# Performance work log

Measured on AMD Instinct MI355X. Metric: run time of the kernel, lower is better.

The kernel has to match this reference:

```python
import jax, jax.numpy as jnp
import numpy as np

B, N = 256, 256


def greedy_hard_perm(soft_perm):
    # soft_perm: (B, N, N). Sequential greedy masked-argmax assignment, vectorized over batch.
    Bn, Nn, _ = soft_perm.shape
    NEG = jnp.finfo(soft_perm.dtype).min
    b_idx = jnp.arange(Bn)

    def step(carry, _):
        scores, hard, row_mask, col_mask = carry
        # mask out already-assigned rows/cols (in-place masked_fill_ in torch -> carried scores)
        scores = jnp.where(row_mask[:, :, None], NEG, scores)
        scores = jnp.where(col_mask[:, None, :], NEG, scores)
        flat_idx = jnp.argmax(scores.reshape(Bn, -1), axis=1)  # (B,)
        r = flat_idx // Nn
        c = flat_idx % Nn
        hard = hard.at[b_idx, r, c].set(1.0)
        row_mask = row_mask.at[b_idx, r].set(True)
        col_mask = col_mask.at[b_idx, c].set(True)
        return (scores, hard, row_mask, col_mask), None

    init = (
        soft_perm,
        jnp.zeros_like(soft_perm),
        jnp.zeros((Bn, Nn), dtype=bool),
        jnp.zeros((Bn, Nn), dtype=bool),
    )
    (_, hard, _, _), _ = jax.lax.scan(step, init, None, length=Nn)
    return hard


def setup_inputs() -> dict:
    key = jax.random.key(0)
    logits = jax.random.normal(key, (B, N, N), dtype=jnp.float32)
    # realistic soft permutation: row-stochastic scores
    soft_perm = jax.nn.softmax(logits, axis=-1)
    return {"soft_perm": soft_perm}


def reference(soft_perm):
    # hard perm carries no gradient (built from constant 1.0 writes in torch)
    hard = greedy_hard_perm(jax.lax.stop_gradient(soft_perm))
    # straight-through estimator: forward = hard, backward = identity through soft
    return hard + soft_perm - jax.lax.stop_gradient(soft_perm)
```

## Files before the change

### kernel.cpp

```cpp
#include <hip/hip_runtime.h>
#include <math.h>

#define NEGINF (-INFINITY)

template <int CTRL>
__device__ __forceinline__ float dppmax(float x) {
    int xi = __float_as_int(x);
    int yi = __builtin_amdgcn_update_dpp(xi, xi, CTRL, 0xf, 0xf, false);
    return fmaxf(x, __int_as_float(yi));
}

__device__ __forceinline__ float wave_max64(float x) {
    x = dppmax<0x111>(x);
    x = dppmax<0x112>(x);
    x = dppmax<0x114>(x);
    x = dppmax<0x118>(x);
    x = dppmax<0x142>(x);
    x = dppmax<0x143>(x);
    return __int_as_float(__builtin_amdgcn_readlane(__float_as_int(x), 63));
}

__device__ __forceinline__ void wave_argmax(float v, int idx, float& out_v, int& out_idx) {
    float mv = wave_max64(v);
    unsigned long long mask = __ballot(v == mv);
    int ln = (int)__builtin_ctzll(mask);
    int bi = __builtin_amdgcn_readlane(idx, ln);
    unsigned long long rest = mask & (mask - 1);
    if (rest) {
        while (rest) {
            int l2 = (int)__builtin_ctzll(rest); rest &= rest - 1;
            int b2 = __builtin_amdgcn_readlane(idx, l2);
            if (b2 < bi) bi = b2;
        }
    }
    out_v = mv; out_idx = bi;
}

__global__ __launch_bounds__(64, 1) void greedy_perm_kernel(
        const float* __restrict__ soft, float* __restrict__ out) {
    const int b = blockIdx.x;
    const int lane = threadIdx.x;
    const size_t base = (size_t)b << 16;
    const float* sc = soft + base;
    float* ob = out + base;

    float v[4];
    int   c[4];

#pragma unroll
    for (int j = 0; j < 4; ++j) { v[j] = NEGINF; c[j] = 0; }

    const float4 zero4 = make_float4(0.f, 0.f, 0.f, 0.f);

    for (int k = 0; k < 64; k += 4) {
        float4 w[4][4];
#pragma unroll
        for (int j = 0; j < 4; ++j) {
            const float4* rp = (const float4*)(sc + (size_t)(j * 64 + lane) * 256);
#pragma unroll
            for (int kk = 0; kk < 4; ++kk) w[j][kk] = rp[k + kk];
        }
#pragma unroll
        for (int j = 0; j < 4; ++j) {
            float4* op = (float4*)(ob + (size_t)(j * 64 + lane) * 256);
#pragma unroll
            for (int kk = 0; kk < 4; ++kk) op[k + kk] = zero4;
        }
#pragma unroll
        for (int j = 0; j < 4; ++j) {
#pragma unroll
            for (int kk = 0; kk < 4; ++kk) {
                const float4 ww = w[j][kk];
                const int bc = 4 * (k + kk);
                if (ww.x > v[j]) { v[j] = ww.x; c[j] = bc + 0; }
                if (ww.y > v[j]) { v[j] = ww.y; c[j] = bc + 1; }
                if (ww.z > v[j]) { v[j] = ww.z; c[j] = bc + 2; }
                if (ww.w > v[j]) { v[j] = ww.w; c[j] = bc + 3; }
            }
        }
    }

    __threadfence_block();

    unsigned int colmask = 0;

    for (int step = 0; step < 256; ++step) {
        float bv = v[0];
        int   bf = (lane << 8) | (c[0] & 255);
#pragma unroll
        for (int j = 1; j < 4; ++j) {
            int f = ((j * 64 + lane) << 8) | (c[j] & 255);
            if (v[j] > bv || (v[j] == bv && f < bf)) { bv = v[j]; bf = f; }
        }
        float gv; int gf;
        wave_argmax(bv, bf, gv, gf);
        const int r  = gf >> 8;
        const int cc = gf & 255;

        if (lane == 0) ob[gf] = 1.0f;
        if (lane == (r & 63)) { v[r >> 6] = NEGINF; c[r >> 6] = 300; }
        if (lane == (cc >> 2)) colmask |= 1u << (cc & 3);

#pragma unroll
        for (int j = 0; j < 4; ++j) {
            unsigned long long m = __ballot(c[j] == cc);
            while (m) {
                const int ln = (int)__builtin_ctzll(m); m &= m - 1;
                const int row = j * 64 + ln;
                float4 w = *(const float4*)(sc + (size_t)row * 256 + lane * 4);
                float m0 = (colmask & 1u) ? NEGINF : w.x;
                float m1 = (colmask & 2u) ? NEGINF : w.y;
                float m2 = (colmask & 4u) ? NEGINF : w.z;
                float m3 = (colmask & 8u) ? NEGINF : w.w;
                float lv = m0; int lf = 4 * lane + 0;
                if (m1 > lv) { lv = m1; lf = 4 * lane + 1; }
                if (m2 > lv) { lv = m2; lf = 4 * lane + 2; }
                if (m3 > lv) { lv = m3; lf = 4 * lane + 3; }
                float rv; int rf;
                wave_argmax(lv, lf, rv, rf);
                if (lane == ln) { v[j] = rv; c[j] = rf; }
            }
        }
    }
}

extern "C" void kernel_launch(void* const* d_in, const int* in_sizes, int n_in,
                              void* d_out, int out_size, void* d_ws, size_t ws_size,
                              hipStream_t stream) {
    const float* soft = (const float*)d_in[0];
    float* out = (float*)d_out;
    const int n_batches = in_sizes[0] >> 16;

    greedy_perm_kernel<<<n_batches, 64, 0, stream>>>(soft, out);
}
```

Before: 321.5 us.

## Pack argmax keys into 64-bit, defer row rescans, cache half the matrix in LDS

Packs each value and its inverted flat index into one 64-bit key, so a wave max gives the argmax with lowest-index tie-breaking and the ballot and readlane tie loop go away. Up to three invalidated rows are rescanned lazily in the next step, so their loads overlap with the next global reduction. The first 128 rows are staged in 128 KB of dynamic LDS with an XOR swizzle so rescans of those rows avoid global memory. Risks: 64-bit DPP reductions double the shuffle count, the large LDS request may fail (there is a fallback), and the key packing drops non-positive values to zero.

```diff
diff --git a/kernel.cpp b/kernel.cpp
--- a/kernel.cpp
+++ b/kernel.cpp
@@ -3,52 +3,70 @@
 
 #define NEGINF (-INFINITY)
 
+typedef unsigned long long u64;
+typedef unsigned int u32;
+
+#define RST 128
+
+
+__device__ __forceinline__ u64 pack_key(float v, int flat) {
+    u64 k = ((u64)__float_as_uint(v) << 32) | (u64)(u32)(0xFFFF ^ flat);
+    return (v > 0.f) ? k : 0ull;
+}
+
 template <int CTRL>
-__device__ __forceinline__ float dppmax(float x) {
-    int xi = __float_as_int(x);
-    int yi = __builtin_amdgcn_update_dpp(xi, xi, CTRL, 0xf, 0xf, false);
-    return fmaxf(x, __int_as_float(yi));
-}
-
-__device__ __forceinline__ float wave_max64(float x) {
-    x = dppmax<0x111>(x);
-    x = dppmax<0x112>(x);
-    x = dppmax<0x114>(x);
-    x = dppmax<0x118>(x);
-    x = dppmax<0x142>(x);
-    x = dppmax<0x143>(x);
-    return __int_as_float(__builtin_amdgcn_readlane(__float_as_int(x), 63));
-}
-
-__device__ __forceinline__ void wave_argmax(float v, int idx, float& out_v, int& out_idx) {
-    float mv = wave_max64(v);
-    unsigned long long mask = __ballot(v == mv);
-    int ln = (int)__builtin_ctzll(mask);
-    int bi = __builtin_amdgcn_readlane(idx, ln);
-    unsigned long long rest = mask & (mask - 1);
-    if (rest) {
-        while (rest) {
-            int l2 = (int)__builtin_ctzll(rest); rest &= rest - 1;
-            int b2 = __builtin_amdgcn_readlane(idx, l2);
-            if (b2 < bi) bi = b2;
-        }
-    }
-    out_v = mv; out_idx = bi;
-}
-
+__device__ __forceinline__ u64 dppmax64(u64 x) {
+    int lo = (int)(u32)x;
+    int hi = (int)(u32)(x >> 32);
+    int ylo = __builtin_amdgcn_update_dpp(lo, lo, CTRL, 0xf, 0xf, false);
+    int yhi = __builtin_amdgcn_update_dpp(hi, hi, CTRL, 0xf, 0xf, false);
+    u64 y = ((u64)(u32)yhi << 32) | (u64)(u32)ylo;
+    return y > x ? y : x;
+}
+
+__device__ __forceinline__ u64 wave_keymax(u64 x) {
+    x = dppmax64<0x111>(x);
+    x = dppmax64<0x112>(x);
+    x = dppmax64<0x114>(x);
+    x = dppmax64<0x118>(x);
+    x = dppmax64<0x142>(x);
+    x = dppmax64<0x143>(x);
+    int lo = __builtin_amdgcn_readlane((int)(u32)x, 63);
+    int hi = __builtin_amdgcn_readlane((int)(u32)(x >> 32), 63);
+    return ((u64)(u32)hi << 32) | (u64)(u32)lo;
+}
+
+__device__ __forceinline__ u64 rescan_finish(int drow, float4 w, u32 colmask,
+                                             int lane, u64 (&key)[4]) {
+    const int base = (drow << 8) | (lane << 2);
+    u64 k = 0, t;
+    t = pack_key(w.x, base + 0); if (!(colmask & 1u) && t > k) k = t;
+    t = pack_key(w.y, base + 1); if (!(colmask & 2u) && t > k) k = t;
+    t = pack_key(w.z, base + 2); if (!(colmask & 4u) && t > k) k = t;
+    t = pack_key(w.w, base + 3); if (!(colmask & 8u) && t > k) k = t;
+    u64 kr = wave_keymax(k);
+    if (lane == (drow & 63)) {
+        const int rj = drow >> 6;
+#pragma unroll
+        for (int j = 0; j < 4; ++j) if (rj == j) key[j] = kr;
+    }
+    return kr;
+}
+
+template <int RSTT>
 __global__ __launch_bounds__(64, 1) void greedy_perm_kernel(
         const float* __restrict__ soft, float* __restrict__ out) {
+    extern __shared__ float smem[];
     const int b = blockIdx.x;
     const int lane = threadIdx.x;
     const size_t base = (size_t)b << 16;
     const float* sc = soft + base;
     float* ob = out + base;
 
-    float v[4];
-    int   c[4];
-
-#pragma unroll
-    for (int j = 0; j < 4; ++j) { v[j] = NEGINF; c[j] = 0; }
+    float vmax[4];
+    int cbest[4];
+#pragma unroll
+    for (int j = 0; j < 4; ++j) { vmax[j] = NEGINF; cbest[j] = 0; }
 
     const float4 zero4 = make_float4(0.f, 0.f, 0.f, 0.f);
 
@@ -65,6 +83,15 @@
             float4* op = (float4*)(ob + (size_t)(j * 64 + lane) * 256);
 #pragma unroll
             for (int kk = 0; kk < 4; ++kk) op[k + kk] = zero4;
+        }
+        if (RSTT > 0) {
+#pragma unroll
+            for (int j = 0; j < 2; ++j) {
+                float* lp = &smem[(j * 64 + lane) << 8];
+#pragma unroll
+                for (int kk = 0; kk < 4; ++kk)
+                    *(float4*)&lp[((k + kk) ^ lane) << 2] = w[j][kk];
+            }
         }
 #pragma unroll
         for (int j = 0; j < 4; ++j) {
@@ -72,53 +99,99 @@
             for (int kk = 0; kk < 4; ++kk) {
                 const float4 ww = w[j][kk];
                 const int bc = 4 * (k + kk);
-                if (ww.x > v[j]) { v[j] = ww.x; c[j] = bc + 0; }
-                if (ww.y > v[j]) { v[j] = ww.y; c[j] = bc + 1; }
-                if (ww.z > v[j]) { v[j] = ww.z; c[j] = bc + 2; }
-                if (ww.w > v[j]) { v[j] = ww.w; c[j] = bc + 3; }
+                if (ww.x > vmax[j]) { vmax[j] = ww.x; cbest[j] = bc + 0; }
+                if (ww.y > vmax[j]) { vmax[j] = ww.y; cbest[j] = bc + 1; }
+                if (ww.z > vmax[j]) { vmax[j] = ww.z; cbest[j] = bc + 2; }
+                if (ww.w > vmax[j]) { vmax[j] = ww.w; cbest[j] = bc + 3; }
             }
         }
     }
 
+    u64 key[4];
+#pragma unroll
+    for (int j = 0; j < 4; ++j)
+        key[j] = pack_key(vmax[j], ((j * 64 + lane) << 8) | cbest[j]);
+
     __threadfence_block();
 
-    unsigned int colmask = 0;
+    u32 colmask = 0;
+    int drow0 = -1, drow1 = -1, drow2 = -1;
+    float4 d0 = zero4, d1 = zero4, d2 = zero4;
 
     for (int step = 0; step < 256; ++step) {
-        float bv = v[0];
-        int   bf = (lane << 8) | (c[0] & 255);
-#pragma unroll
-        for (int j = 1; j < 4; ++j) {
-            int f = ((j * 64 + lane) << 8) | (c[j] & 255);
-            if (v[j] > bv || (v[j] == bv && f < bf)) { bv = v[j]; bf = f; }
-        }
-        float gv; int gf;
-        wave_argmax(bv, bf, gv, gf);
+        u64 ka = key[0] > key[1] ? key[0] : key[1];
+        u64 kb = key[2] > key[3] ? key[2] : key[3];
+        u64 kw = wave_keymax(ka > kb ? ka : kb);
+
+        if (drow0 >= 0) {
+            u64 kr = rescan_finish(drow0, d0, colmask, lane, key);
+            if (kr > kw) kw = kr;
+            drow0 = -1;
+        }
+        if (drow1 >= 0) {
+            u64 kr = rescan_finish(drow1, d1, colmask, lane, key);
+            if (kr > kw) kw = kr;
+            drow1 = -1;
+        }
+        if (drow2 >= 0) {
+            u64 kr = rescan_finish(drow2, d2, colmask, lane, key);
+            if (kr > kw) kw = kr;
+            drow2 = -1;
+        }
+
+        const int gf = 0xFFFF ^ (int)(u32)(kw & 0xFFFFull);
         const int r  = gf >> 8;
         const int cc = gf & 255;
-
         if (lane == 0) ob[gf] = 1.0f;
-        if (lane == (r & 63)) { v[r >> 6] = NEGINF; c[r >> 6] = 300; }
+        {
+            const bool amr = (lane == (r & 63));
+            const int rj = r >> 6;
+#pragma unroll
+            for (int j = 0; j < 4; ++j) if (amr && rj == j) key[j] = 0;
+        }
         if (lane == (cc >> 2)) colmask |= 1u << (cc & 3);
 
-#pragma unroll
-        for (int j = 0; j < 4; ++j) {
-            unsigned long long m = __ballot(c[j] == cc);
+        const u32 lowb = (u32)(0xFF ^ cc);
+        u64 bm[4];
+#pragma unroll
+        for (int j = 0; j < 4; ++j) {
+            const bool dj = (key[j] > 0xFFFFull) && (((u32)key[j] & 0xFFu) == lowb);
+            bm[j] = __ballot(dj);
+        }
+
+        int nass = 0;
+#pragma unroll
+        for (int j = 0; j < 4; ++j) {
+            u64 m = bm[j];
             while (m) {
                 const int ln = (int)__builtin_ctzll(m); m &= m - 1;
                 const int row = j * 64 + ln;
-                float4 w = *(const float4*)(sc + (size_t)row * 256 + lane * 4);
-                float m0 = (colmask & 1u) ? NEGINF : w.x;
-                float m1 = (colmask & 2u) ? NEGINF : w.y;
-                float m2 = (colmask & 4u) ? NEGINF : w.z;
-                float m3 = (colmask & 8u) ? NEGINF : w.w;
-                float lv = m0; int lf = 4 * lane + 0;
-                if (m1 > lv) { lv = m1; lf = 4 * lane + 1; }
-                if (m2 > lv) { lv = m2; lf = 4 * lane + 2; }
-                if (m3 > lv) { lv = m3; lf = 4 * lane + 3; }
-                float rv; int rf;
-                wave_argmax(lv, lf, rv, rf);
-                if (lane == ln) { v[j] = rv; c[j] = rf; }
+                if (nass == 0) {
+                    drow0 = row;
+                    d0 = (RSTT > 0 && row < RSTT)
+                        ? *(const float4*)&smem[(row << 8) | (((lane ^ ln) & 63) << 2)]
+                        : *(const float4*)(sc + ((size_t)row << 8) + (lane << 2));
+                } else if (nass == 1) {
+                    drow1 = row;
+                    d1 = (RSTT > 0 && row < RSTT)
+                        ? *(const float4*)&smem[(row << 8) | (((lane ^ ln) & 63) << 2)]
+                        : *(const float4*)(sc + ((size_t)row << 8) + (lane << 2));
+                } else if (nass == 2) {
+                    drow2 = row;
+                    d2 = (RSTT > 0 && row < RSTT)
+                        ? *(const float4*)&smem[(row << 8) | (((lane ^ ln) & 63) << 2)]
+                        : *(const float4*)(sc + ((size_t)row << 8) + (lane << 2));
+                } else {
+                    float4 w = (RSTT > 0 && row < RSTT)
+                        ? *(const float4*)&smem[(row << 8) | (((lane ^ ln) & 63) << 2)]
+                        : *(const float4*)(sc + ((size_t)row << 8) + (lane << 2));
+                    rescan_finish(row, w, colmask, lane, key);
+                }
+                if (nass < 3 && lane == ln) {
+#pragma unroll
+                    for (int jj = 0; jj < 4; ++jj) if (jj == j) key[jj] = 0;
+                }
+                ++nass;
             }
         }
     }
@@ -131,5 +204,15 @@
     float* out = (float*)d_out;
     const int n_batches = in_sizes[0] >> 16;
 
-    greedy_perm_kernel<<<n_batches, 64, 0, stream>>>(soft, out);
-}
+    static int use_lds = -1;
+    if (use_lds < 0) {
+        hipError_t e = hipFuncSetAttribute(
+            reinterpret_cast<const void*>(greedy_perm_kernel<RST>),
+            hipFuncAttributeMaxDynamicSharedMemorySize, RST * 256 * 4);
+        use_lds = (e == hipSuccess) ? 1 : 0;
+    }
+    if (use_lds)
+        greedy_perm_kernel<RST><<<n_batches, 64, RST * 256 * 4, stream>>>(soft, out);
+    else
+        greedy_perm_kernel<0><<<n_batches, 64, 0, stream>>>(soft, out);
+}
```

Result: slower. 454.0 us (+41.2%).

## Defer stale-row rescans via slotted prefetch buffers to hide load latency

Applied to the files above, without the earlier changes.

Rows whose cached max column was just taken are no longer rescanned at once with a blocking global load. Their data is prefetched into one of four register slots and the row is marked stale (sentinel 256). A stale row is only rescanned when it wins the argmax or when its slot has aged two steps. This overlaps global load latency with later greedy steps on the serial critical path, at the cost of extra control flow, retry loops and register pressure.

```diff
diff --git a/kernel.cpp b/kernel.cpp
--- a/kernel.cpp
+++ b/kernel.cpp
@@ -2,6 +2,9 @@
 #include <math.h>
 
 #define NEGINF (-INFINITY)
+
+typedef unsigned int u32;
+typedef unsigned long long u64;
 
 template <int CTRL>
 __device__ __forceinline__ float dppmax(float x) {
@@ -36,6 +39,25 @@
     out_v = mv; out_idx = bi;
 }
 
+__device__ __forceinline__ void consume_row(int row, float4 w, u32 colmask, int lane,
+                                            float (&rv)[4], int (&rc)[4]) {
+    float m0 = (colmask & 1u) ? NEGINF : w.x;
+    float m1 = (colmask & 2u) ? NEGINF : w.y;
+    float m2 = (colmask & 4u) ? NEGINF : w.z;
+    float m3 = (colmask & 8u) ? NEGINF : w.w;
+    float lv = m0; int lf = 4 * lane;
+    if (m1 > lv) { lv = m1; lf = 4 * lane + 1; }
+    if (m2 > lv) { lv = m2; lf = 4 * lane + 2; }
+    if (m3 > lv) { lv = m3; lf = 4 * lane + 3; }
+    float nv; int nc;
+    wave_argmax(lv, lf, nv, nc);
+    if (lane == (row & 63)) {
+        const int rj = row >> 6;
+#pragma unroll
+        for (int j = 0; j < 4; ++j) if (j == rj) { rv[j] = nv; rc[j] = nc; }
+    }
+}
+
 __global__ __launch_bounds__(64, 1) void greedy_perm_kernel(
         const float* __restrict__ soft, float* __restrict__ out) {
     const int b = blockIdx.x;
@@ -44,11 +66,10 @@
     const float* sc = soft + base;
     float* ob = out + base;
 
-    float v[4];
-    int   c[4];
-
+    float rv[4];
+    int   rc[4];
 #pragma unroll
-    for (int j = 0; j < 4; ++j) { v[j] = NEGINF; c[j] = 0; }
+    for (int j = 0; j < 4; ++j) { rv[j] = NEGINF; rc[j] = 0; }
 
     const float4 zero4 = make_float4(0.f, 0.f, 0.f, 0.f);
 
@@ -72,54 +93,85 @@
             for (int kk = 0; kk < 4; ++kk) {
                 const float4 ww = w[j][kk];
                 const int bc = 4 * (k + kk);
-                if (ww.x > v[j]) { v[j] = ww.x; c[j] = bc + 0; }
-                if (ww.y > v[j]) { v[j] = ww.y; c[j] = bc + 1; }
-                if (ww.z > v[j]) { v[j] = ww.z; c[j] = bc + 2; }
-                if (ww.w > v[j]) { v[j] = ww.w; c[j] = bc + 3; }
+                if (ww.x > rv[j]) { rv[j] = ww.x; rc[j] = bc + 0; }
+                if (ww.y > rv[j]) { rv[j] = ww.y; rc[j] = bc + 1; }
+                if (ww.z > rv[j]) { rv[j] = ww.z; rc[j] = bc + 2; }
+                if (ww.w > rv[j]) { rv[j] = ww.w; rc[j] = bc + 3; }
             }
         }
     }
 
     __threadfence_block();
 
-    unsigned int colmask = 0;
+    u32 colmask = 0;
+
+    float4 d0 = zero4, d1 = zero4, d2 = zero4, d3 = zero4;
+    int sr0 = -1, sr1 = -1, sr2 = -1, sr3 = -1;
+    int age0 = 0, age1 = 0, age2 = 0, age3 = 0;
 
     for (int step = 0; step < 256; ++step) {
-        float bv = v[0];
-        int   bf = (lane << 8) | (c[0] & 255);
+        float gv; int gf, r, cc;
+        for (;;) {
+            float bv = rv[0]; int bf = (lane << 8) | (rc[0] & 255);
 #pragma unroll
-        for (int j = 1; j < 4; ++j) {
-            int f = ((j * 64 + lane) << 8) | (c[j] & 255);
-            if (v[j] > bv || (v[j] == bv && f < bf)) { bv = v[j]; bf = f; }
+            for (int j = 1; j < 4; ++j) {
+                const float vj = rv[j];
+                const int   fj = (((j << 6) + lane) << 8) | (rc[j] & 255);
+                if (vj > bv || (vj == bv && fj < bf)) { bv = vj; bf = fj; }
+            }
+            wave_argmax(bv, bf, gv, gf);
+            r  = gf >> 8;
+            cc = gf & 255;
+            const int rj = r >> 6;
+            int myc = rc[0];
+#pragma unroll
+            for (int j = 1; j < 4; ++j) if (j == rj) myc = rc[j];
+            const int wc = __builtin_amdgcn_readlane(myc, r & 63);
+            if (wc < 256) break;
+            if      (sr0 == r) { consume_row(r, d0, colmask, lane, rv, rc); sr0 = -1; }
+            else if (sr1 == r) { consume_row(r, d1, colmask, lane, rv, rc); sr1 = -1; }
+            else if (sr2 == r) { consume_row(r, d2, colmask, lane, rv, rc); sr2 = -1; }
+            else               { consume_row(r, d3, colmask, lane, rv, rc); sr3 = -1; }
         }
-        float gv; int gf;
-        wave_argmax(bv, bf, gv, gf);
-        const int r  = gf >> 8;
-        const int cc = gf & 255;
 
         if (lane == 0) ob[gf] = 1.0f;
-        if (lane == (r & 63)) { v[r >> 6] = NEGINF; c[r >> 6] = 300; }
+        if (lane == (r & 63)) {
+            const int rj = r >> 6;
+#pragma unroll
+            for (int j = 0; j < 4; ++j) if (j == rj) { rv[j] = NEGINF; rc[j] = 257; }
+        }
         if (lane == (cc >> 2)) colmask |= 1u << (cc & 3);
 
 #pragma unroll
         for (int j = 0; j < 4; ++j) {
-            unsigned long long m = __ballot(c[j] == cc);
+            u64 m = __ballot(rc[j] == cc);
             while (m) {
                 const int ln = (int)__builtin_ctzll(m); m &= m - 1;
-                const int row = j * 64 + ln;
-                float4 w = *(const float4*)(sc + (size_t)row * 256 + lane * 4);
-                float m0 = (colmask & 1u) ? NEGINF : w.x;
-                float m1 = (colmask & 2u) ? NEGINF : w.y;
-                float m2 = (colmask & 4u) ? NEGINF : w.z;
-                float m3 = (colmask & 8u) ? NEGINF : w.w;
-                float lv = m0; int lf = 4 * lane + 0;
-                if (m1 > lv) { lv = m1; lf = 4 * lane + 1; }
-                if (m2 > lv) { lv = m2; lf = 4 * lane + 2; }
-                if (m3 > lv) { lv = m3; lf = 4 * lane + 3; }
-                float rv; int rf;
-                wave_argmax(lv, lf, rv, rf);
-                if (lane == ln) { v[j] = rv; c[j] = rf; }
+                const int row = (j << 6) + ln;
+                if (lane == ln) rc[j] = 256;
+                const float4* rp = (const float4*)(sc + ((size_t)row << 8)) + lane;
+                if      (sr0 < 0) { d0 = *rp; sr0 = row; age0 = 0; }
+                else if (sr1 < 0) { d1 = *rp; sr1 = row; age1 = 0; }
+                else if (sr2 < 0) { d2 = *rp; sr2 = row; age2 = 0; }
+                else if (sr3 < 0) { d3 = *rp; sr3 = row; age3 = 0; }
+                else {
+                    float4 w = *rp;
+                    consume_row(row, w, colmask, lane, rv, rc);
+                }
             }
+        }
+
+        ++age0; ++age1; ++age2; ++age3;
+        if      (sr0 >= 0 && age0 >= 2) { consume_row(sr0, d0, colmask, lane, rv, rc); sr0 = -1; }
+        else if (sr1 >= 0 && age1 >= 2) { consume_row(sr1, d1, colmask, lane, rv, rc); sr1 = -1; }
+        else if (sr2 >= 0 && age2 >= 2) { consume_row(sr2, d2, colmask, lane, rv, rc); sr2 = -1; }
+        else if (sr3 >= 0 && age3 >= 2) { consume_row(sr3, d3, colmask, lane, rv, rc); sr3 = -1; }
+        const int occ = (sr0 >= 0) + (sr1 >= 0) + (sr2 >= 0) + (sr3 >= 0);
+        if (occ >= 3) {
+            if      (sr0 >= 0 && age0 >= 2) { consume_row(sr0, d0, colmask, lane, rv, rc); sr0 = -1; }
+            else if (sr1 >= 0 && age1 >= 2) { consume_row(sr1, d1, colmask, lane, rv, rc); sr1 = -1; }
+            else if (sr2 >= 0 && age2 >= 2) { consume_row(sr2, d2, colmask, lane, rv, rc); sr2 = -1; }
+            else if (sr3 >= 0 && age3 >= 2) { consume_row(sr3, d3, colmask, lane, rv, rc); sr3 = -1; }
         }
     }
 }
```

Result: slower. 555.7 us (+72.8%).

## Track second-best per row and cache first 128 rows in LDS

Applied to the files above, without the earlier changes.

Each row now keeps its best and second-best column, so when its best column is taken it can fall back to the second-best without rescanning the row. A rescan now finds both top-1 and top-2. The first 128 rows of the batch matrix are stored in 128 KB of dynamic shared memory with a swizzled layout, so rescans of those rows read LDS instead of global memory. The cost is more registers, a large LDS footprint with a fallback path when the attribute cannot be set, and a second wave reduction on every rescan.

```diff
diff --git a/kernel.cpp b/kernel.cpp
--- a/kernel.cpp
+++ b/kernel.cpp
@@ -2,6 +2,11 @@
 #include <math.h>
 
 #define NEGINF (-INFINITY)
+
+typedef unsigned int u32;
+typedef unsigned long long u64;
+
+#define RST 128
 
 template <int CTRL>
 __device__ __forceinline__ float dppmax(float x) {
@@ -22,10 +27,10 @@
 
 __device__ __forceinline__ void wave_argmax(float v, int idx, float& out_v, int& out_idx) {
     float mv = wave_max64(v);
-    unsigned long long mask = __ballot(v == mv);
+    u64 mask = __ballot(v == mv);
     int ln = (int)__builtin_ctzll(mask);
     int bi = __builtin_amdgcn_readlane(idx, ln);
-    unsigned long long rest = mask & (mask - 1);
+    u64 rest = mask & (mask - 1);
     if (rest) {
         while (rest) {
             int l2 = (int)__builtin_ctzll(rest); rest &= rest - 1;
@@ -36,19 +41,20 @@
     out_v = mv; out_idx = bi;
 }
 
+template <int RSTT>
 __global__ __launch_bounds__(64, 1) void greedy_perm_kernel(
         const float* __restrict__ soft, float* __restrict__ out) {
+    extern __shared__ float smem[];
     const int b = blockIdx.x;
     const int lane = threadIdx.x;
     const size_t base = (size_t)b << 16;
     const float* sc = soft + base;
     float* ob = out + base;
 
-    float v[4];
-    int   c[4];
-
-#pragma unroll
-    for (int j = 0; j < 4; ++j) { v[j] = NEGINF; c[j] = 0; }
+    float rv[4], sv[4];
+    int   rc[4], scc[4];
+#pragma unroll
+    for (int j = 0; j < 4; ++j) { rv[j] = NEGINF; rc[j] = 0; sv[j] = NEGINF; scc[j] = 300; }
 
     const float4 zero4 = make_float4(0.f, 0.f, 0.f, 0.f);
 
@@ -65,6 +71,15 @@
             float4* op = (float4*)(ob + (size_t)(j * 64 + lane) * 256);
 #pragma unroll
             for (int kk = 0; kk < 4; ++kk) op[k + kk] = zero4;
+        }
+        if (RSTT > 0) {
+#pragma unroll
+            for (int j = 0; j < 2; ++j) {
+                float* lp = &smem[(j * 64 + lane) << 8];
+#pragma unroll
+                for (int kk = 0; kk < 4; ++kk)
+                    *(float4*)&lp[((k + kk) ^ lane) << 2] = w[j][kk];
+            }
         }
 #pragma unroll
         for (int j = 0; j < 4; ++j) {
@@ -72,25 +87,34 @@
             for (int kk = 0; kk < 4; ++kk) {
                 const float4 ww = w[j][kk];
                 const int bc = 4 * (k + kk);
-                if (ww.x > v[j]) { v[j] = ww.x; c[j] = bc + 0; }
-                if (ww.y > v[j]) { v[j] = ww.y; c[j] = bc + 1; }
-                if (ww.z > v[j]) { v[j] = ww.z; c[j] = bc + 2; }
-                if (ww.w > v[j]) { v[j] = ww.w; c[j] = bc + 3; }
+                const float e[4] = {ww.x, ww.y, ww.z, ww.w};
+#pragma unroll
+                for (int q = 0; q < 4; ++q) {
+                    const float x = e[q];
+                    const int   cx = bc + q;
+                    const bool g1 = x > rv[j];
+                    const bool g2 = x > sv[j];
+                    sv[j]  = g1 ? rv[j] : (g2 ? x  : sv[j]);
+                    scc[j] = g1 ? rc[j] : (g2 ? cx : scc[j]);
+                    rv[j]  = g1 ? x  : rv[j];
+                    rc[j]  = g1 ? cx : rc[j];
+                }
             }
         }
     }
 
     __threadfence_block();
 
-    unsigned int colmask = 0;
+    u32 colmask = 0;
 
     for (int step = 0; step < 256; ++step) {
-        float bv = v[0];
-        int   bf = (lane << 8) | (c[0] & 255);
+        float bv = rv[0];
+        int   bf = (lane << 8) | (rc[0] & 255);
 #pragma unroll
         for (int j = 1; j < 4; ++j) {
-            int f = ((j * 64 + lane) << 8) | (c[j] & 255);
-            if (v[j] > bv || (v[j] == bv && f < bf)) { bv = v[j]; bf = f; }
+            const float vj = rv[j];
+            const int   fj = (((j << 6) + lane) << 8) | (rc[j] & 255);
+            if (vj > bv || (vj == bv && fj < bf)) { bv = vj; bf = fj; }
         }
         float gv; int gf;
         wave_argmax(bv, bf, gv, gf);
@@ -98,27 +122,60 @@
         const int cc = gf & 255;
 
         if (lane == 0) ob[gf] = 1.0f;
-        if (lane == (r & 63)) { v[r >> 6] = NEGINF; c[r >> 6] = 300; }
+        if (lane == (r & 63)) {
+            const int rj = r >> 6;
+#pragma unroll
+            for (int j = 0; j < 4; ++j) if (j == rj) { rv[j] = NEGINF; rc[j] = 300; }
+        }
         if (lane == (cc >> 2)) colmask |= 1u << (cc & 3);
 
 #pragma unroll
-        for (int j = 0; j < 4; ++j) {
-            unsigned long long m = __ballot(c[j] == cc);
+        for (int j = 0; j < 4; ++j) if (scc[j] == cc) scc[j] = 300;
+
+#pragma unroll
+        for (int j = 0; j < 4; ++j) {
+            const bool dirty = (rc[j] == cc);
+            const bool need  = dirty && (scc[j] == 300);
+            if (dirty && !need) {
+                rv[j] = sv[j]; rc[j] = scc[j];
+                sv[j] = NEGINF; scc[j] = 300;
+            }
+            u64 m = __ballot(need);
             while (m) {
                 const int ln = (int)__builtin_ctzll(m); m &= m - 1;
-                const int row = j * 64 + ln;
-                float4 w = *(const float4*)(sc + (size_t)row * 256 + lane * 4);
+                const int row = (j << 6) + ln;
+                float4 w = (RSTT > 0 && row < RSTT)
+                    ? *(const float4*)&smem[(row << 8) | (((lane ^ ln) & 63) << 2)]
+                    : *(const float4*)(sc + ((size_t)row << 8) + (lane << 2));
                 float m0 = (colmask & 1u) ? NEGINF : w.x;
                 float m1 = (colmask & 2u) ? NEGINF : w.y;
                 float m2 = (colmask & 4u) ? NEGINF : w.z;
                 float m3 = (colmask & 8u) ? NEGINF : w.w;
-                float lv = m0; int lf = 4 * lane + 0;
+                float lv = m0; int lf = 4 * lane;
                 if (m1 > lv) { lv = m1; lf = 4 * lane + 1; }
                 if (m2 > lv) { lv = m2; lf = 4 * lane + 2; }
                 if (m3 > lv) { lv = m3; lf = 4 * lane + 3; }
-                float rv; int rf;
-                wave_argmax(lv, lf, rv, rf);
-                if (lane == ln) { v[j] = rv; c[j] = rf; }
+                float nv; int nc;
+                wave_argmax(lv, lf, nv, nc);
+                const bool wl = (lane == (nc >> 2));
+                if (wl && (nc & 3) == 0) m0 = NEGINF;
+                if (wl && (nc & 3) == 1) m1 = NEGINF;
+                if (wl && (nc & 3) == 2) m2 = NEGINF;
+                if (wl && (nc & 3) == 3) m3 = NEGINF;
+                float lv2 = m0; int lf2 = 4 * lane;
+                if (m1 > lv2) { lv2 = m1; lf2 = 4 * lane + 1; }
+                if (m2 > lv2) { lv2 = m2; lf2 = 4 * lane + 2; }
+                if (m3 > lv2) { lv2 = m3; lf2 = 4 * lane + 3; }
+                float nv2; int nc2;
+                wave_argmax(lv2, lf2, nv2, nc2);
+                if (lane == ln) {
+#pragma unroll
+                    for (int jj = 0; jj < 4; ++jj) if (jj == j) {
+                        rv[jj] = nv; rc[jj] = nc;
+                        sv[jj]  = nv2;
+                        scc[jj] = (nv2 > 0.f) ? nc2 : 300;
+                    }
+                }
             }
         }
     }
@@ -131,5 +188,15 @@
     float* out = (float*)d_out;
     const int n_batches = in_sizes[0] >> 16;
 
-    greedy_perm_kernel<<<n_batches, 64, 0, stream>>>(soft, out);
-}
+    static int use_lds = -1;
+    if (use_lds < 0) {
+        hipError_t e = hipFuncSetAttribute(
+            reinterpret_cast<const void*>(greedy_perm_kernel<RST>),
+            hipFuncAttributeMaxDynamicSharedMemorySize, RST * 256 * 4);
+        use_lds = (e == hipSuccess) ? 1 : 0;
+    }
+    if (use_lds)
+        greedy_perm_kernel<RST><<<n_batches, 64, RST * 256 * 4, stream>>>(soft, out);
+    else
+        greedy_perm_kernel<0><<<n_batches, 64, 0, stream>>>(soft, out);
+}
```

New measurement: 342.6 us. +6.6%, slower.
